# Optimization experiments

Measured on AMD Instinct MI355X. Metric: run time of the kernel, lower is better.

## Reference

```python
import jax, jax.numpy as jnp
import numpy as np
import math

H = 1024
E = 16
ENT_STRENGTH = 0.5
COHERENCE_TIME = 10.0
TIME_STEP = 0.0
K = 2
# static list of rotation pairs (i<j), applied sequentially as in the torch double loop
PAIRS = np.array([(i, j) for i in range(E) for j in range(i + 1, E)], dtype=np.int32)


def _mlp(x, w1, b1, w2, b2):
    h = jax.nn.gelu(x @ w1 + b1, approximate=False)  # torch default GELU = exact erf
    return h @ w2 + b2


def _apply_entanglement(amps, ent):
    # sequential Givens rotations over expert pairs; carry shape [B,S,E]
    pairs = jnp.asarray(PAIRS)

    def step(carry, pair):
        i, j = pair[0], pair[1]
        angle = ent[i, j] * ENT_STRENGTH
        c, s = jnp.cos(angle), jnp.sin(angle)
        ai = jnp.take(carry, i, axis=-1)  # [B,S]
        aj = jnp.take(carry, j, axis=-1)
        oh_i = jax.nn.one_hot(i, E, dtype=carry.dtype)
        oh_j = jax.nn.one_hot(j, E, dtype=carry.dtype)
        new = (carry * (1.0 - oh_i - oh_j)
               + (c * ai - s * aj)[..., None] * oh_i
               + (s * ai + c * aj)[..., None] * oh_j)
        return new, None

    out, _ = jax.lax.scan(step, amps, pairs)
    return out


def setup_inputs() -> dict:
    key = jax.random.key(0)
    ks = jax.random.split(key, 10)
    sc1 = 1.0 / math.sqrt(H)
    sc2 = 1.0 / math.sqrt(H // 2)
    return {
        "hidden_states": jax.random.normal(ks[0], (4, 4096, H), dtype=jnp.float32),
        "w1a": jax.random.uniform(ks[1], (H, H // 2), jnp.float32, -sc1, sc1),
        "b1a": jnp.zeros((H // 2,), jnp.float32),
        "w2a": jax.random.uniform(ks[2], (H // 2, E), jnp.float32, -sc2, sc2),
        "b2a": jnp.zeros((E,), jnp.float32),
        "w1p": jax.random.uniform(ks[3], (H, H // 2), jnp.float32, -sc1, sc1),
        "b1p": jnp.zeros((H // 2,), jnp.float32),
        "w2p": jax.random.uniform(ks[4], (H // 2, E), jnp.float32, -sc2, sc2),
        "b2p": jnp.zeros((E,), jnp.float32),
        "ent": jax.random.normal(ks[5], (E, E), dtype=jnp.float32) * 0.1,
    }


def reference(hidden_states, w1a, b1a, w2a, b2a, w1p, b1p, w2p, b2p, ent):
    raw_amps = _mlp(hidden_states, w1a, b1a, w2a, b2a)                 # [B,S,E]
    raw_phases = jnp.tanh(_mlp(hidden_states, w1p, b1p, w2p, b2p)) * jnp.float32(math.pi)
    amplitudes = jnp.sqrt(jax.nn.softmax(jnp.abs(raw_amps), axis=-1))
    entangled = _apply_entanglement(amplitudes, ent)
    coherence = jnp.exp(jnp.float32(-TIME_STEP / COHERENCE_TIME))      # time_step buffer = 0 -> 1.0
    decoherent = entangled * coherence
    probs = decoherent ** 2
    probs = probs / jnp.maximum(jnp.sum(jnp.abs(probs), axis=-1, keepdims=True), 1e-12)
    top_p, top_i = jax.lax.top_k(probs, K)
    top_p = top_p / jnp.maximum(jnp.sum(jnp.abs(top_p), axis=-1, keepdims=True), 1e-12)
    return top_p, top_i, decoherent, raw_phases, probs
```

## Files before the change

### kernel.cpp

```cpp
#include <hip/hip_runtime.h>
#include <math.h>

#define NTOK   16384
#define HDIM   1024
#define HHALF  512
#define NE     16

#define OFF_TP  0
#define OFF_TI  (NTOK * 2)
#define OFF_DEC (NTOK * 4)
#define OFF_PH  (OFF_DEC + NTOK * NE)
#define OFF_PR  (OFF_PH + NTOK * NE)

typedef _Float16 half8 __attribute__((ext_vector_type(8)));
typedef _Float16 half4 __attribute__((ext_vector_type(4)));
typedef float f32x16 __attribute__((ext_vector_type(16)));
typedef float f32x4 __attribute__((ext_vector_type(4)));

#define LO_SCALE     2048.0f
#define LO_SCALE_INV (1.0f / 2048.0f)
#define MFMA32(a,b,c) __builtin_amdgcn_mfma_f32_32x32x16_f16(a,b,c,0,0,0)
#define MFMA16(a,b,c) __builtin_amdgcn_mfma_f32_16x16x32_f16(a,b,c,0,0,0)

#define BAR() asm volatile("s_waitcnt lgkmcnt(0)\n\ts_barrier" ::: "memory")

__device__ __forceinline__ float gelu_exact(float x) {
    return 0.5f * x * (1.0f + erff(x * 0.70710678118654752440f));
}

__device__ __forceinline__ void cvt_split(float4 v, half4& hi, half4& lo) {
    _Float16 h0 = (_Float16)v.x, h1 = (_Float16)v.y,
             h2 = (_Float16)v.z, h3 = (_Float16)v.w;
    hi = (half4){h0, h1, h2, h3};
    lo = (half4){(_Float16)((v.x - (float)h0) * LO_SCALE),
                 (_Float16)((v.y - (float)h1) * LO_SCALE),
                 (_Float16)((v.z - (float)h2) * LO_SCALE),
                 (_Float16)((v.w - (float)h3) * LO_SCALE)};
}

__global__ void __launch_bounds__(256)
qir_wtrans(const float* __restrict__ w1a, const float* __restrict__ w1p,
           _Float16* __restrict__ wt, float* __restrict__ out)
{
    int u = blockIdx.x * 256 + threadIdx.x;
    out[OFF_PH + u] = 0.0f;
    out[OFF_PH + 262144 + u] = 0.0f;

    int l  = u & 63;
    int f  = (u >> 6) & 7;
    int sl = (u >> 9) & 7;
    int kc = (u >> 12) & 31;
    int ph = u >> 17;
    int nf = f >> 2, kh = (f >> 1) & 1, pl = f & 1;
    int col = sl * 64 + nf * 32 + (l & 31);
    int k0  = kc * 32 + kh * 16 + (l >> 5) * 8;
    const float* __restrict__ W = ph ? w1p : w1a;
    half8 v;
    #pragma unroll
    for (int j = 0; j < 8; ++j) {
        float x = W[(size_t)(k0 + j) * HHALF + col];
        _Float16 h = (_Float16)x;
        v[j] = pl ? (_Float16)((x - (float)h) * LO_SCALE) : h;
    }
    *(half8*)&wt[(size_t)u * 8] = v;
}

__device__ __forceinline__ void kstep(
    int kc, const float* __restrict__ aptr, const _Float16* __restrict__ bptr,
    char* Acur, char* Anxt, int a_rd, int a_off0, int a_off1,
    half8 (&Bc)[8], half8 (&Bn)[8],
    float4 (&xw)[2], float4 (&xl)[2],
    f32x16& a00, f32x16& a01, f32x16& a10, f32x16& a11,
    f32x16& c00, f32x16& c01, f32x16& c10, f32x16& c11)
{
    if (kc + 2 < 32) {
        xl[0] = *(const float4*)(aptr + (kc + 2) * 32);
        xl[1] = *(const float4*)(aptr + (kc + 2) * 32 + 16);
    }
    if (kc + 1 < 32) {
        #pragma unroll
        for (int f = 0; f < 8; ++f)
            Bn[f] = *(const half8*)(bptr + (size_t)(kc + 1) * 32768 + f * 512);
    }
    #pragma unroll
    for (int kh = 0; kh < 2; ++kh) {
        const char* Ah = Acur + kh * 2048 + a_rd;
        half8 ah0 = *(const half8*)(Ah);
        half8 ah1 = *(const half8*)(Ah + 512);
        half8 al0 = *(const half8*)(Ah + 4096);
        half8 al1 = *(const half8*)(Ah + 4096 + 512);
        half8 bh0 = Bc[kh * 2],     bl0 = Bc[kh * 2 + 1];
        half8 bh1 = Bc[4 + kh * 2], bl1 = Bc[4 + kh * 2 + 1];
        a00 = MFMA32(ah0, bh0, a00); c00 = MFMA32(al0, bh0, c00); c00 = MFMA32(ah0, bl0, c00);
        a01 = MFMA32(ah0, bh1, a01); c01 = MFMA32(al0, bh1, c01); c01 = MFMA32(ah0, bl1, c01);
        a10 = MFMA32(ah1, bh0, a10); c10 = MFMA32(al1, bh0, c10); c10 = MFMA32(ah1, bl0, c10);
        a11 = MFMA32(ah1, bh1, a11); c11 = MFMA32(al1, bh1, c11); c11 = MFMA32(ah1, bl1, c11);
    }
    if (kc + 1 < 32) {
        half4 hv, lv;
        cvt_split(xw[0], hv, lv);
        *(half4*)(Anxt + a_off0) = hv; *(half4*)(Anxt + a_off0 + 4096) = lv;
        cvt_split(xw[1], hv, lv);
        *(half4*)(Anxt + a_off1) = hv; *(half4*)(Anxt + a_off1 + 4096) = lv;
    }
    BAR();
}

__global__ void __launch_bounds__(256, 2)
qir_gemm(const float* __restrict__ xg, const _Float16* __restrict__ wt,
         const float* __restrict__ b1a, const float* __restrict__ w2a, const float* __restrict__ b2a,
         const float* __restrict__ b1p, const float* __restrict__ w2p, const float* __restrict__ b2p,
         float* __restrict__ out)
{
    extern __shared__ char smem[];
    const int tid = threadIdx.x;
    const int l  = tid & 63;
    const int w  = tid >> 6;
    const int bid  = blockIdx.x;
    const int mblk = bid & 255;
    const int v    = bid >> 8;
    const int ph   = v & 1;
    const int nh   = v >> 1;
    const int tok0 = mblk * 64;

    const float* __restrict__ b1 = ph ? b1p : b1a;
    const float* __restrict__ w2 = ph ? w2p : w2a;
    const float* __restrict__ b2 = ph ? b2p : b2a;
    const _Float16* __restrict__ wtp = wt + ((size_t)ph << 20);

    char* const Ab0 = smem;
    char* const Ab1 = smem + 8192;

    const int r  = tid >> 2;
    const int kq = tid & 3;
    const float* __restrict__ aptr = xg + (size_t)(tok0 + r) * HDIM + kq * 4;
    const int a_off0 = (kq >> 1) * 1024 + r * 16 + (kq & 1) * 8;
    const int a_off1 = a_off0 + 2048;
    const int a_rd = (l >> 5) * 1024 + (l & 31) * 16;

    const _Float16* __restrict__ bptr = wtp + (nh * 4 + w) * 4096 + (size_t)l * 8;

    f32x16 a00{}, a01{}, a10{}, a11{}, c00{}, c01{}, c10{}, c11{};
    #pragma unroll
    for (int rg = 0; rg < 16; ++rg) {
        a00[rg] = 0.f; a01[rg] = 0.f; a10[rg] = 0.f; a11[rg] = 0.f;
        c00[rg] = 0.f; c01[rg] = 0.f; c10[rg] = 0.f; c11[rg] = 0.f;
    }

    half8 Bc[8], Bn[8];
    float4 xw[2], xl[2];

    {
        float4 v0 = *(const float4*)(aptr);
        float4 v1 = *(const float4*)(aptr + 16);
        half4 hv, lv;
        cvt_split(v0, hv, lv);
        *(half4*)(Ab0 + a_off0) = hv; *(half4*)(Ab0 + a_off0 + 4096) = lv;
        cvt_split(v1, hv, lv);
        *(half4*)(Ab0 + a_off1) = hv; *(half4*)(Ab0 + a_off1 + 4096) = lv;
    }
    #pragma unroll
    for (int f = 0; f < 8; ++f) Bc[f] = *(const half8*)(bptr + f * 512);
    xw[0] = *(const float4*)(aptr + 32);
    xw[1] = *(const float4*)(aptr + 48);
    BAR();

    for (int kk = 0; kk < 16; ++kk) {
        kstep(2 * kk,     aptr, bptr, Ab0, Ab1, a_rd, a_off0, a_off1,
              Bc, Bn, xw, xl, a00, a01, a10, a11, c00, c01, c10, c11);
        kstep(2 * kk + 1, aptr, bptr, Ab1, Ab0, a_rd, a_off0, a_off1,
              Bn, Bc, xl, xw, a00, a01, a10, a11, c00, c01, c10, c11);
    }

    const int col0 = nh * 256 + w * 64 + (l & 31);
    const float bb0 = b1[col0], bb1 = b1[col0 + 32];
    #pragma unroll
    for (int rg = 0; rg < 16; ++rg) {
        a00[rg] = gelu_exact(a00[rg] + c00[rg] * LO_SCALE_INV + bb0);
        a01[rg] = gelu_exact(a01[rg] + c01[rg] * LO_SCALE_INV + bb1);
        a10[rg] = gelu_exact(a10[rg] + c10[rg] * LO_SCALE_INV + bb0);
        a11[rg] = gelu_exact(a11[rg] + c11[rg] * LO_SCALE_INV + bb1);
    }

    char* const Hw = smem + w * 4096;
    char* const hb = Hw + ((l >> 3) & 3) * 1024 + (l & 7) * 2;
    float* const P = (float*)(smem + 16384);

    half8 w2h[2], w2l[2];
    #pragma unroll
    for (int nf = 0; nf < 2; ++nf) {
        #pragma unroll
        for (int j = 0; j < 8; ++j) {
            int kg = nh * 256 + w * 64 + nf * 32 + (l >> 4) * 8 + j;
            float vv = w2[(size_t)kg * NE + (l & 15)];
            _Float16 hh = (_Float16)vv;
            w2h[nf][j] = hh;
            w2l[nf][j] = (_Float16)((vv - (float)hh) * LO_SCALE);
        }
    }

    f32x4 acc2[4], acc2s[4];
    #pragma unroll
    for (int m16 = 0; m16 < 4; ++m16)
        #pragma unroll
        for (int rg = 0; rg < 4; ++rg) { acc2[m16][rg] = 0.f; acc2s[m16][rg] = 0.f; }

#define H2PASS(ACC0, ACC1, NF, PL)                                             \
    {                                                                          \
        _Pragma("unroll")                                                      \
        for (int rg = 0; rg < 16; ++rg) {                                      \
            int row0 = (rg & 3) + 8 * (rg >> 2) + 4 * (l >> 5);                \
            { float vv = ACC0[rg]; _Float16 hh = (_Float16)vv;                 \
              *(_Float16*)(hb + row0 * 16) =                                   \
                  (PL) ? (_Float16)(vv - (float)hh) : hh; }                    \
            { float vv = ACC1[rg]; _Float16 hh = (_Float16)vv;                 \
              *(_Float16*)(hb + (32 + row0) * 16) =                            \
                  (PL) ? (_Float16)(vv - (float)hh) : hh; }                    \
        }                                                                      \
        _Pragma("unroll")                                                      \
        for (int m16 = 0; m16 < 4; ++m16) {                                    \
            half8 a2 = *(const half8*)(Hw + (l >> 4) * 1024 +                  \
                                       (m16 * 16 + (l & 15)) * 16);            \
            acc2[m16] = MFMA16(a2, w2h[NF], acc2[m16]);                        \
            if (!(PL)) acc2s[m16] = MFMA16(a2, w2l[NF], acc2s[m16]);           \
        }                                                                      \
    }

    H2PASS(a00, a10, 0, 0)
    H2PASS(a01, a11, 1, 0)
    H2PASS(a00, a10, 0, 1)
    H2PASS(a01, a11, 1, 1)
#undef H2PASS

    #pragma unroll
    for (int m16 = 0; m16 < 4; ++m16)
        #pragma unroll
        for (int rg = 0; rg < 4; ++rg) {
            int row = m16 * 16 + ((l >> 4) << 2) + rg;
            P[w * 1024 + row * 16 + (l & 15)] =
                acc2[m16][rg] + acc2s[m16][rg] * LO_SCALE_INV;
        }
    __syncthreads();

    #pragma unroll
    for (int rep = 0; rep < 4; ++rep) {
        int oi = tid + rep * 256;
        int t = oi >> 4, e = oi & 15;
        float sum = 0.5f * b2[e]
                  + P[0 * 1024 + t * 16 + e]
                  + P[1 * 1024 + t * 16 + e]
                  + P[2 * 1024 + t * 16 + e]
                  + P[3 * 1024 + t * 16 + e];
        atomicAdd(out + (ph ? OFF_PH : OFF_PR) + (size_t)(tok0 + t) * NE + e, sum);
    }
}

__global__ void __launch_bounds__(512)
qir_mlp(const float* __restrict__ xg,
        const float* __restrict__ w1a, const float* __restrict__ b1a,
        const float* __restrict__ w2a, const float* __restrict__ b2a,
        const float* __restrict__ w1p, const float* __restrict__ b1p,
        const float* __restrict__ w2p, const float* __restrict__ b2p,
        float* __restrict__ out)
{
    __shared__ float sh_w[16][HHALF];
    __shared__ float sh_x[16][68];

    const int tid  = threadIdx.x;
    const int cg   = tid & 63;
    const int tg   = tid >> 6;
    const int tok0 = blockIdx.x * 64;
    const int cA   = cg * 4;
    const int cB   = 256 + cg * 4;

    for (int phase = 0; phase < 2; ++phase) {
        const float* __restrict__ w1 = phase ? w1p : w1a;
        const float* __restrict__ b1 = phase ? b1p : b1a;
        const float* __restrict__ w2 = phase ? w2p : w2a;
        const float* __restrict__ b2 = phase ? b2p : b2a;

        float acc[8][8];
        #pragma unroll
        for (int t = 0; t < 8; ++t)
            #pragma unroll
            for (int c = 0; c < 8; ++c) acc[t][c] = 0.0f;

        float4 wreg[4];
        float4 xreg = make_float4(0.f, 0.f, 0.f, 0.f);

        auto load_chunk = [&](int kc) {
            #pragma unroll
            for (int p = 0; p < 4; ++p) {
                int f  = tid + p * 512;
                int k  = f >> 7;
                int c4 = (f & 127) << 2;
                wreg[p] = *(const float4*)&w1[(kc * 16 + k) * HHALF + c4];
            }
            if (tid < 256) {
                int t  = tid >> 2;
                int k4 = (tid & 3) << 2;
                xreg = *(const float4*)&xg[(size_t)(tok0 + t) * HDIM + kc * 16 + k4];
            }
        };

        load_chunk(0);
        for (int kc = 0; kc < HDIM / 16; ++kc) {
            __syncthreads();
            #pragma unroll
            for (int p = 0; p < 4; ++p) {
                int f  = tid + p * 512;
                int k  = f >> 7;
                int c4 = (f & 127) << 2;
                *(float4*)&sh_w[k][c4] = wreg[p];
            }
            if (tid < 256) {
                int t  = tid >> 2;
                int k4 = (tid & 3) << 2;
                sh_x[k4 + 0][t] = xreg.x;
                sh_x[k4 + 1][t] = xreg.y;
                sh_x[k4 + 2][t] = xreg.z;
                sh_x[k4 + 3][t] = xreg.w;
            }
            __syncthreads();
            if (kc + 1 < HDIM / 16) load_chunk(kc + 1);

            #pragma unroll 4
            for (int k = 0; k < 16; ++k) {
                float4 xa = *(const float4*)&sh_x[k][tg * 8];
                float4 xb = *(const float4*)&sh_x[k][tg * 8 + 4];
                float4 wa = *(const float4*)&sh_w[k][cA];
                float4 wb = *(const float4*)&sh_w[k][cB];
                float xs[8] = {xa.x, xa.y, xa.z, xa.w, xb.x, xb.y, xb.z, xb.w};
                float ws[8] = {wa.x, wa.y, wa.z, wa.w, wb.x, wb.y, wb.z, wb.w};
                #pragma unroll
                for (int t = 0; t < 8; ++t)
                    #pragma unroll
                    for (int c = 0; c < 8; ++c)
                        acc[t][c] = fmaf(xs[t], ws[c], acc[t][c]);
            }
        }

        {
            float4 bA4 = *(const float4*)&b1[cA];
            float4 bB4 = *(const float4*)&b1[cB];
            float bs[8] = {bA4.x, bA4.y, bA4.z, bA4.w, bB4.x, bB4.y, bB4.z, bB4.w};
            #pragma unroll
            for (int t = 0; t < 8; ++t)
                #pragma unroll
                for (int c = 0; c < 8; ++c)
                    acc[t][c] = gelu_exact(acc[t][c] + bs[c]);
        }

        for (int e = 0; e < NE; ++e) {
            float w2v[8];
            #pragma unroll
            for (int j = 0; j < 4; ++j) {
                w2v[j]     = w2[(cA + j) * NE + e];
                w2v[4 + j] = w2[(cB + j) * NE + e];
            }
            float bias2 = b2[e];
            #pragma unroll
            for (int t = 0; t < 8; ++t) {
                float s = 0.0f;
                #pragma unroll
                for (int j = 0; j < 8; ++j) s = fmaf(acc[t][j], w2v[j], s);
                #pragma unroll
                for (int off = 1; off < 64; off <<= 1)
                    s += __shfl_xor(s, off, 64);
                if (cg == 0) {
                    float raw   = s + bias2;
                    int   token = tok0 + tg * 8 + t;
                    out[(phase ? OFF_PH : OFF_PR) + (size_t)token * NE + e] = raw;
                }
            }
        }
    }
}

__global__ void __launch_bounds__(256)
qir_epilogue(const float* __restrict__ ent, float* __restrict__ out)
{
    __shared__ float sh_c[120], sh_s[120];
    const int tid = threadIdx.x;
    if (tid < 120) {
        int rem = tid, i = 0;
        while (rem >= 15 - i) { rem -= 15 - i; ++i; }
        int j = i + 1 + rem;
        float ang = ent[i * NE + j] * 0.5f;
        sh_c[tid] = cosf(ang);
        sh_s[tid] = sinf(ang);
    }
    __syncthreads();

    const int token = blockIdx.x * 256 + tid;

    #pragma unroll
    for (int q = 0; q < 4; ++q) {
        float4 v = *(const float4*)&out[OFF_PH + (size_t)token * NE + q * 4];
        v.x = tanhf(v.x) * 3.14159265358979323846f;
        v.y = tanhf(v.y) * 3.14159265358979323846f;
        v.z = tanhf(v.z) * 3.14159265358979323846f;
        v.w = tanhf(v.w) * 3.14159265358979323846f;
        *(float4*)&out[OFF_PH + (size_t)token * NE + q * 4] = v;
    }

    float a[16];
    #pragma unroll
    for (int q = 0; q < 4; ++q) {
        float4 v = *(const float4*)&out[OFF_PR + (size_t)token * NE + q * 4];
        a[q*4+0] = v.x; a[q*4+1] = v.y; a[q*4+2] = v.z; a[q*4+3] = v.w;
    }

    float m = fabsf(a[0]);
    #pragma unroll
    for (int e = 1; e < 16; ++e) m = fmaxf(m, fabsf(a[e]));
    float ssum = 0.0f;
    #pragma unroll
    for (int e = 0; e < 16; ++e) { a[e] = expf(fabsf(a[e]) - m); ssum += a[e]; }
    float inv = 1.0f / ssum;
    #pragma unroll
    for (int e = 0; e < 16; ++e) a[e] = sqrtf(a[e] * inv);

    {
        int p = 0;
        #pragma unroll
        for (int i = 0; i < 16; ++i) {
            #pragma unroll
            for (int j = i + 1; j < 16; ++j) {
                float c = sh_c[p], s = sh_s[p]; ++p;
                float ai = a[i], aj = a[j];
                a[i] = c * ai - s * aj;
                a[j] = s * ai + c * aj;
            }
        }
    }

    #pragma unroll
    for (int q = 0; q < 4; ++q)
        *(float4*)&out[OFF_DEC + (size_t)token * NE + q * 4] =
            make_float4(a[q*4], a[q*4+1], a[q*4+2], a[q*4+3]);

    float pr[16];
    float s2 = 0.0f;
    #pragma unroll
    for (int e = 0; e < 16; ++e) { pr[e] = a[e] * a[e]; s2 += pr[e]; }
    float inv2 = 1.0f / fmaxf(s2, 1e-12f);
    #pragma unroll
    for (int e = 0; e < 16; ++e) pr[e] *= inv2;
    #pragma unroll
    for (int q = 0; q < 4; ++q)
        *(float4*)&out[OFF_PR + (size_t)token * NE + q * 4] =
            make_float4(pr[q*4], pr[q*4+1], pr[q*4+2], pr[q*4+3]);

    float bv = pr[0]; int bi = 0;
    #pragma unroll
    for (int e = 1; e < 16; ++e) if (pr[e] > bv) { bv = pr[e]; bi = e; }
    float sv = -1.0f; int si = 0;
    #pragma unroll
    for (int e = 0; e < 16; ++e) if (e != bi && pr[e] > sv) { sv = pr[e]; si = e; }
    float ts = fmaxf(fabsf(bv) + fabsf(sv), 1e-12f);
    out[OFF_TP + (size_t)token * 2 + 0] = bv / ts;
    out[OFF_TP + (size_t)token * 2 + 1] = sv / ts;
    out[OFF_TI + (size_t)token * 2 + 0] = (float)bi;
    out[OFF_TI + (size_t)token * 2 + 1] = (float)si;
}

extern "C" void kernel_launch(void* const* d_in, const int* in_sizes, int n_in,
                              void* d_out, int out_size, void* d_ws, size_t ws_size,
                              hipStream_t stream) {
    const float* xg  = (const float*)d_in[0];
    const float* w1a = (const float*)d_in[1];
    const float* b1a = (const float*)d_in[2];
    const float* w2a = (const float*)d_in[3];
    const float* b2a = (const float*)d_in[4];
    const float* w1p = (const float*)d_in[5];
    const float* b1p = (const float*)d_in[6];
    const float* w2p = (const float*)d_in[7];
    const float* b2p = (const float*)d_in[8];
    const float* ent = (const float*)d_in[9];
    float* out = (float*)d_out;

    if (ws_size >= (size_t)4 * 1024 * 1024) {
        _Float16* wt = (_Float16*)d_ws;
        qir_wtrans<<<1024, 256, 0, stream>>>(w1a, w1p, wt, out);
        qir_gemm<<<1024, 256, 32768, stream>>>(xg, wt, b1a, w2a, b2a,
                                               b1p, w2p, b2p, out);
    } else {
        qir_mlp<<<NTOK / 64, 512, 0, stream>>>(xg, w1a, b1a, w2a, b2a,
                                               w1p, b1p, w2p, b2p, out);
    }
    qir_epilogue<<<NTOK / 256, 256, 0, stream>>>(ent, out);
}
```

Baseline: 125.9 us.

## Replace split-f16 GEMM scheme with f16/bf16 three-term product and narrower tiles

The first-layer GEMM changes its error-compensated split. Instead of hi/lo f16 terms on both operands with separate accumulators, it uses the x hi and scaled lo parts times the W f16 hi, plus a bf16 x-hi times a bf16 W residual. Everything accumulates into a single scaled accumulator pair per wave, and the lo-times-lo and separate correction accumulators are dropped. Each block now covers 32 columns per wave instead of 64, so the grid doubles to 2048 blocks, occupancy rises to 3 blocks per CU, and register pressure drops. The risks are reduced precision from the bf16 residual term and more total A-tile conversion and LDS traffic per output.

```diff
diff --git a/kernel.cpp b/kernel.cpp
--- a/kernel.cpp
+++ b/kernel.cpp
@@ -5,6 +5,7 @@
 #define HDIM   1024
 #define HHALF  512
 #define NE     16
+#define PI_F   3.14159265358979323846f
 
 #define OFF_TP  0
 #define OFF_TI  (NTOK * 2)
@@ -14,33 +15,31 @@
 
 typedef _Float16 half8 __attribute__((ext_vector_type(8)));
 typedef _Float16 half4 __attribute__((ext_vector_type(4)));
+typedef short    bf8   __attribute__((ext_vector_type(8)));
+typedef short    bf4   __attribute__((ext_vector_type(4)));
 typedef float f32x16 __attribute__((ext_vector_type(16)));
 typedef float f32x4 __attribute__((ext_vector_type(4)));
 
-#define LO_SCALE     2048.0f
-#define LO_SCALE_INV (1.0f / 2048.0f)
-#define MFMA32(a,b,c) __builtin_amdgcn_mfma_f32_32x32x16_f16(a,b,c,0,0,0)
-#define MFMA16(a,b,c) __builtin_amdgcn_mfma_f32_16x16x32_f16(a,b,c,0,0,0)
+#define SCALE      2048.0f
+#define SCALE_INV  (1.0f / 2048.0f)
+#define MFMA_F16(a,b,c)  __builtin_amdgcn_mfma_f32_32x32x16_f16(a,b,c,0,0,0)
+#define MFMA_BF16(a,b,c) __builtin_amdgcn_mfma_f32_32x32x16_bf16(a,b,c,0,0,0)
+#define MFMA16(a,b,c)    __builtin_amdgcn_mfma_f32_16x16x32_f16(a,b,c,0,0,0)
 
 #define BAR() asm volatile("s_waitcnt lgkmcnt(0)\n\ts_barrier" ::: "memory")
 
 __device__ __forceinline__ float gelu_exact(float x) {
     return 0.5f * x * (1.0f + erff(x * 0.70710678118654752440f));
 }
-
-__device__ __forceinline__ void cvt_split(float4 v, half4& hi, half4& lo) {
-    _Float16 h0 = (_Float16)v.x, h1 = (_Float16)v.y,
-             h2 = (_Float16)v.z, h3 = (_Float16)v.w;
-    hi = (half4){h0, h1, h2, h3};
-    lo = (half4){(_Float16)((v.x - (float)h0) * LO_SCALE),
-                 (_Float16)((v.y - (float)h1) * LO_SCALE),
-                 (_Float16)((v.z - (float)h2) * LO_SCALE),
-                 (_Float16)((v.w - (float)h3) * LO_SCALE)};
+__device__ __forceinline__ short f32_to_bf16_bits(float f) {
+    unsigned u = __builtin_bit_cast(unsigned, f);
+    u += 0x7FFFu + ((u >> 16) & 1u);
+    return (short)(u >> 16);
 }
 
 __global__ void __launch_bounds__(256)
 qir_wtrans(const float* __restrict__ w1a, const float* __restrict__ w1p,
-           _Float16* __restrict__ wt, float* __restrict__ out)
+           short* __restrict__ wt, float* __restrict__ out)
 {
     int u = blockIdx.x * 256 + threadIdx.x;
     out[OFF_PH + u] = 0.0f;
@@ -55,23 +54,23 @@
     int col = sl * 64 + nf * 32 + (l & 31);
     int k0  = kc * 32 + kh * 16 + (l >> 5) * 8;
     const float* __restrict__ W = ph ? w1p : w1a;
-    half8 v;
+    bf8 v;
     #pragma unroll
     for (int j = 0; j < 8; ++j) {
         float x = W[(size_t)(k0 + j) * HHALF + col];
         _Float16 h = (_Float16)x;
-        v[j] = pl ? (_Float16)((x - (float)h) * LO_SCALE) : h;
-    }
-    *(half8*)&wt[(size_t)u * 8] = v;
+        v[j] = pl ? f32_to_bf16_bits(x - (float)h)
+                  : __builtin_bit_cast(short, h);
+    }
+    *(bf8*)&wt[(size_t)u * 8] = v;
 }
 
 __device__ __forceinline__ void kstep(
-    int kc, const float* __restrict__ aptr, const _Float16* __restrict__ bptr,
-    char* Acur, char* Anxt, int a_rd, int a_off0, int a_off1,
-    half8 (&Bc)[8], half8 (&Bn)[8],
+    int kc, const float* __restrict__ aptr, const short* __restrict__ bptr,
+    char* Acur, char* Anxt, int a_rd, int a_w0,
+    bf8 (&Bc)[4], bf8 (&Bn)[4],
     float4 (&xw)[2], float4 (&xl)[2],
-    f32x16& a00, f32x16& a01, f32x16& a10, f32x16& a11,
-    f32x16& c00, f32x16& c01, f32x16& c10, f32x16& c11)
+    f32x16& acc0, f32x16& acc1)
 {
     if (kc + 2 < 32) {
         xl[0] = *(const float4*)(aptr + (kc + 2) * 32);
@@ -79,35 +78,55 @@
     }
     if (kc + 1 < 32) {
         #pragma unroll
-        for (int f = 0; f < 8; ++f)
-            Bn[f] = *(const half8*)(bptr + (size_t)(kc + 1) * 32768 + f * 512);
+        for (int j = 0; j < 4; ++j)
+            Bn[j] = *(const bf8*)(bptr + (size_t)(kc + 1) * 32768 + j * 512);
     }
     #pragma unroll
     for (int kh = 0; kh < 2; ++kh) {
-        const char* Ah = Acur + kh * 2048 + a_rd;
-        half8 ah0 = *(const half8*)(Ah);
-        half8 ah1 = *(const half8*)(Ah + 512);
-        half8 al0 = *(const half8*)(Ah + 4096);
-        half8 al1 = *(const half8*)(Ah + 4096 + 512);
-        half8 bh0 = Bc[kh * 2],     bl0 = Bc[kh * 2 + 1];
-        half8 bh1 = Bc[4 + kh * 2], bl1 = Bc[4 + kh * 2 + 1];
-        a00 = MFMA32(ah0, bh0, a00); c00 = MFMA32(al0, bh0, c00); c00 = MFMA32(ah0, bl0, c00);
-        a01 = MFMA32(ah0, bh1, a01); c01 = MFMA32(al0, bh1, c01); c01 = MFMA32(ah0, bl1, c01);
-        a10 = MFMA32(ah1, bh0, a10); c10 = MFMA32(al1, bh0, c10); c10 = MFMA32(ah1, bl0, c10);
-        a11 = MFMA32(ah1, bh1, a11); c11 = MFMA32(al1, bh1, c11); c11 = MFMA32(ah1, bl1, c11);
+        const char* Ah = Acur + kh * 6144 + a_rd;
+        half8 xh0 = *(const half8*)(Ah);
+        half8 xh1 = *(const half8*)(Ah + 512);
+        half8 xl0 = *(const half8*)(Ah + 1024);
+        half8 xl1 = *(const half8*)(Ah + 1536);
+        bf8   xb0 = *(const bf8*)  (Ah + 2048);
+        bf8   xb1 = *(const bf8*)  (Ah + 2560);
+        half8 wh  = __builtin_bit_cast(half8, Bc[kh * 2]);
+        bf8   wlo = Bc[kh * 2 + 1];
+        acc0 = MFMA_F16(xh0, wh, acc0);
+        acc1 = MFMA_F16(xh1, wh, acc1);
+        acc0 = MFMA_F16(xl0, wh, acc0);
+        acc1 = MFMA_F16(xl1, wh, acc1);
+        acc0 = MFMA_BF16(xb0, wlo, acc0);
+        acc1 = MFMA_BF16(xb1, wlo, acc1);
     }
     if (kc + 1 < 32) {
-        half4 hv, lv;
-        cvt_split(xw[0], hv, lv);
-        *(half4*)(Anxt + a_off0) = hv; *(half4*)(Anxt + a_off0 + 4096) = lv;
-        cvt_split(xw[1], hv, lv);
-        *(half4*)(Anxt + a_off1) = hv; *(half4*)(Anxt + a_off1 + 4096) = lv;
+        #pragma unroll
+        for (int kh = 0; kh < 2; ++kh) {
+            float4 v = kh ? xw[1] : xw[0];
+            _Float16 h0 = (_Float16)v.x, h1 = (_Float16)v.y,
+                     h2 = (_Float16)v.z, h3 = (_Float16)v.w;
+            const _Float16 S = (_Float16)SCALE;
+            half4 hi = {(_Float16)(h0 * S), (_Float16)(h1 * S),
+                        (_Float16)(h2 * S), (_Float16)(h3 * S)};
+            half4 lo = {(_Float16)((v.x - (float)h0) * SCALE),
+                        (_Float16)((v.y - (float)h1) * SCALE),
+                        (_Float16)((v.z - (float)h2) * SCALE),
+                        (_Float16)((v.w - (float)h3) * SCALE)};
+            bf4 hb = {f32_to_bf16_bits((float)h0 * SCALE),
+                      f32_to_bf16_bits((float)h1 * SCALE),
+                      f32_to_bf16_bits((float)h2 * SCALE),
+                      f32_to_bf16_bits((float)h3 * SCALE)};
+            char* base = Anxt + kh * 6144 + a_w0;
+            *(half4*)(base)        = hi;
+            *(half4*)(base + 1024) = lo;
+            *(bf4*)  (base + 2048) = hb;
+        }
     }
     BAR();
 }
 
-__global__ void __launch_bounds__(256, 2)
-qir_gemm(const float* __restrict__ xg, const _Float16* __restrict__ wt,
+__global__ void __launch_bounds__(256, 3)
+qir_gemm(const float* __restrict__ xg, const short* __restrict__ wt,
          const float* __restrict__ b1a, const float* __restrict__ w2a, const float* __restrict__ b2a,
          const float* __restrict__ b1p, const float* __restrict__ w2p, const float* __restrict__ b2p,
          float* __restrict__ out)
@@ -126,77 +145,83 @@
     const float* __restrict__ b1 = ph ? b1p : b1a;
     const float* __restrict__ w2 = ph ? w2p : w2a;
     const float* __restrict__ b2 = ph ? b2p : b2a;
-    const _Float16* __restrict__ wtp = wt + ((size_t)ph << 20);
+    const short* __restrict__ wtp = wt + ((size_t)ph << 20);
 
     char* const Ab0 = smem;
-    char* const Ab1 = smem + 8192;
+    char* const Ab1 = smem + 12288;
 
     const int r  = tid >> 2;
     const int kq = tid & 3;
     const float* __restrict__ aptr = xg + (size_t)(tok0 + r) * HDIM + kq * 4;
-    const int a_off0 = (kq >> 1) * 1024 + r * 16 + (kq & 1) * 8;
-    const int a_off1 = a_off0 + 2048;
-    const int a_rd = (l >> 5) * 1024 + (l & 31) * 16;
-
-    const _Float16* __restrict__ bptr = wtp + (nh * 4 + w) * 4096 + (size_t)l * 8;
-
-    f32x16 a00{}, a01{}, a10{}, a11{}, c00{}, c01{}, c10{}, c11{};
-    #pragma unroll
-    for (int rg = 0; rg < 16; ++rg) {
-        a00[rg] = 0.f; a01[rg] = 0.f; a10[rg] = 0.f; a11[rg] = 0.f;
-        c00[rg] = 0.f; c01[rg] = 0.f; c10[rg] = 0.f; c11[rg] = 0.f;
-    }
-
-    half8 Bc[8], Bn[8];
-    float4 xw[2], xl[2];
+    const int a_w0 = (kq >> 1) * 3072 + r * 16 + (kq & 1) * 8;
+    const int a_rd = (l >> 5) * 3072 + (l & 31) * 16;
+
+    const int c32 = nh * 4 + w;
+    const short* __restrict__ bptr =
+        wtp + ((size_t)(c32 >> 1) * 8 + (size_t)(c32 & 1) * 4) * 512 + (size_t)l * 8;
+
+    f32x16 acc0{}, acc1{};
+    #pragma unroll
+    for (int rg = 0; rg < 16; ++rg) { acc0[rg] = 0.f; acc1[rg] = 0.f; }
+
+    bf8 Bc[4], Bn[4];
+    float4 xw[2], xl4[2];
 
     {
-        float4 v0 = *(const float4*)(aptr);
-        float4 v1 = *(const float4*)(aptr + 16);
-        half4 hv, lv;
-        cvt_split(v0, hv, lv);
-        *(half4*)(Ab0 + a_off0) = hv; *(half4*)(Ab0 + a_off0 + 4096) = lv;
-        cvt_split(v1, hv, lv);
-        *(half4*)(Ab0 + a_off1) = hv; *(half4*)(Ab0 + a_off1 + 4096) = lv;
-    }
-    #pragma unroll
-    for (int f = 0; f < 8; ++f) Bc[f] = *(const half8*)(bptr + f * 512);
+        #pragma unroll
+        for (int kh = 0; kh < 2; ++kh) {
+            float4 vv = *(const float4*)(aptr + kh * 16);
+            _Float16 h0 = (_Float16)vv.x, h1 = (_Float16)vv.y,
+                     h2 = (_Float16)vv.z, h3 = (_Float16)vv.w;
+            const _Float16 S = (_Float16)SCALE;
+            half4 hi = {(_Float16)(h0 * S), (_Float16)(h1 * S),
+                        (_Float16)(h2 * S), (_Float16)(h3 * S)};
+            half4 lo = {(_Float16)((vv.x - (float)h0) * SCALE),
+                        (_Float16)((vv.y - (float)h1) * SCALE),
+                        (_Float16)((vv.z - (float)h2) * SCALE),
+                        (_Float16)((vv.w - (float)h3) * SCALE)};
+            bf4 hb = {f32_to_bf16_bits((float)h0 * SCALE),
+                      f32_to_bf16_bits((float)h1 * SCALE),
+                      f32_to_bf16_bits((float)h2 * SCALE),
+                      f32_to_bf16_bits((float)h3 * SCALE)};
+            char* base = Ab0 + kh * 6144 + a_w0;
+            *(half4*)(base)        = hi;
+            *(half4*)(base + 1024) = lo;
+            *(bf4*)  (base + 2048) = hb;
+        }
+    }
+    #pragma unroll
+    for (int j = 0; j < 4; ++j) Bc[j] = *(const bf8*)(bptr + j * 512);
     xw[0] = *(const float4*)(aptr + 32);
     xw[1] = *(const float4*)(aptr + 48);
     BAR();
 
     for (int kk = 0; kk < 16; ++kk) {
-        kstep(2 * kk,     aptr, bptr, Ab0, Ab1, a_rd, a_off0, a_off1,
-              Bc, Bn, xw, xl, a00, a01, a10, a11, c00, c01, c10, c11);
-        kstep(2 * kk + 1, aptr, bptr, Ab1, Ab0, a_rd, a_off0, a_off1,
-              Bn, Bc, xl, xw, a00, a01, a10, a11, c00, c01, c10, c11);
-    }
-
-    const int col0 = nh * 256 + w * 64 + (l & 31);
-    const float bb0 = b1[col0], bb1 = b1[col0 + 32];
+        kstep(2 * kk,     aptr, bptr, Ab0, Ab1, a_rd, a_w0,
+              Bc, Bn, xw, xl4, acc0, acc1);
+        kstep(2 * kk + 1, aptr, bptr, Ab1, Ab0, a_rd, a_w0,
+              Bn, Bc, xl4, xw, acc0, acc1);
+    }
+
+    const float bb = b1[nh * 128 + w * 32 + (l & 31)];
     #pragma unroll
     for (int rg = 0; rg < 16; ++rg) {
-        a00[rg] = gelu_exact(a00[rg] + c00[rg] * LO_SCALE_INV + bb0);
-        a01[rg] = gelu_exact(a01[rg] + c01[rg] * LO_SCALE_INV + bb1);
-        a10[rg] = gelu_exact(a10[rg] + c10[rg] * LO_SCALE_INV + bb0);
-        a11[rg] = gelu_exact(a11[rg] + c11[rg] * LO_SCALE_INV + bb1);
+        acc0[rg] = gelu_exact(acc0[rg] * SCALE_INV + bb);
+        acc1[rg] = gelu_exact(acc1[rg] * SCALE_INV + bb);
     }
 
     char* const Hw = smem + w * 4096;
     char* const hb = Hw + ((l >> 3) & 3) * 1024 + (l & 7) * 2;
     float* const P = (float*)(smem + 16384);
 
-    half8 w2h[2], w2l[2];
-    #pragma unroll
-    for (int nf = 0; nf < 2; ++nf) {
-        #pragma unroll
-        for (int j = 0; j < 8; ++j) {
-            int kg = nh * 256 + w * 64 + nf * 32 + (l >> 4) * 8 + j;
-            float vv = w2[(size_t)kg * NE + (l & 15)];
-            _Float16 hh = (_Float16)vv;
-            w2h[nf][j] = hh;
-            w2l[nf][j] = (_Float16)((vv - (float)hh) * LO_SCALE);
-        }
+    half8 w2h, w2l;
+    #pragma unroll
+    for (int j = 0; j < 8; ++j) {
+        int kg = nh * 128 + w * 32 + (l >> 4) * 8 + j;
+        float vv = w2[(size_t)kg * NE + (l & 15)];
+        _Float16 hh = (_Float16)vv;
+        w2h[j] = hh;
+        w2l[j] = (_Float16)((vv - (float)hh) * SCALE);
     }
 
     f32x4 acc2[4], acc2s[4];
@@ -205,32 +230,33 @@
         #pragma unroll
         for (int rg = 0; rg < 4; ++rg) { acc2[m16][rg] = 0.f; acc2s[m16][rg] = 0.f; }
 
-#define H2PASS(ACC0, ACC1, NF, PL)                                             \
-    {                                                                          \
-        _Pragma("unroll")                                                      \
-        for (int rg = 0; rg < 16; ++rg) {                                      \
-            int row0 = (rg & 3) + 8 * (rg >> 2) + 4 * (l >> 5);                \
-            { float vv = ACC0[rg]; _Float16 hh = (_Float16)vv;                 \
-              *(_Float16*)(hb + row0 * 16) =                                   \
-                  (PL) ? (_Float16)(vv - (float)hh) : hh; }                    \
-            { float vv = ACC1[rg]; _Float16 hh = (_Float16)vv;                 \
-              *(_Float16*)(hb + (32 + row0) * 16) =                            \
-                  (PL) ? (_Float16)(vv - (float)hh) : hh; }                    \
-        }                                                                      \
-        _Pragma("unroll")                                                      \
-        for (int m16 = 0; m16 < 4; ++m16) {                                    \
-            half8 a2 = *(const half8*)(Hw + (l >> 4) * 1024 +                  \
-                                       (m16 * 16 + (l & 15)) * 16);            \
-            acc2[m16] = MFMA16(a2, w2h[NF], acc2[m16]);                        \
-            if (!(PL)) acc2s[m16] = MFMA16(a2, w2l[NF], acc2s[m16]);           \
-        }                                                                      \
-    }
-
-    H2PASS(a00, a10, 0, 0)
-    H2PASS(a01, a11, 1, 0)
-    H2PASS(a00, a10, 0, 1)
-    H2PASS(a01, a11, 1, 1)
-#undef H2PASS
+    #pragma unroll
+    for (int rg = 0; rg < 16; ++rg) {
+        int row0 = (rg & 3) + 8 * (rg >> 2) + 4 * (l >> 5);
+        *(_Float16*)(hb + row0 * 16)        = (_Float16)acc0[rg];
+        *(_Float16*)(hb + (32 + row0) * 16) = (_Float16)acc1[rg];
+    }
+    #pragma unroll
+    for (int m16 = 0; m16 < 4; ++m16) {
+        half8 a2 = *(const half8*)(Hw + (l >> 4) * 1024 +
+                                   (m16 * 16 + (l & 15)) * 16);
+        acc2[m16]  = MFMA16(a2, w2h, acc2[m16]);
+        acc2s[m16] = MFMA16(a2, w2l, acc2s[m16]);
+    }
+    #pragma unroll
+    for (int rg = 0; rg < 16; ++rg) {
+        int row0 = (rg & 3) + 8 * (rg >> 2) + 4 * (l >> 5);
+        { float vv = acc0[rg]; _Float16 hh = (_Float16)vv;
+          *(_Float16*)(hb + row0 * 16) = (_Float16)(vv - (float)hh); }
+        { float vv = acc1[rg]; _Float16 hh = (_Float16)vv;
+          *(_Float16*)(hb + (32 + row0) * 16) = (_Float16)(vv - (float)hh); }
+    }
+    #pragma unroll
+    for (int m16 = 0; m16 < 4; ++m16) {
+        half8 a2 = *(const half8*)(Hw + (l >> 4) * 1024 +
+                                   (m16 * 16 + (l & 15)) * 16);
+        acc2[m16] = MFMA16(a2, w2h, acc2[m16]);
+    }
 
     #pragma unroll
     for (int m16 = 0; m16 < 4; ++m16)
@@ -238,7 +264,7 @@
         for (int rg = 0; rg < 4; ++rg) {
             int row = m16 * 16 + ((l >> 4) << 2) + rg;
             P[w * 1024 + row * 16 + (l & 15)] =
-                acc2[m16][rg] + acc2s[m16][rg] * LO_SCALE_INV;
+                acc2[m16][rg] + acc2s[m16][rg] * SCALE_INV;
         }
     __syncthreads();
 
@@ -246,7 +272,7 @@
     for (int rep = 0; rep < 4; ++rep) {
         int oi = tid + rep * 256;
         int t = oi >> 4, e = oi & 15;
-        float sum = 0.5f * b2[e]
+        float sum = 0.25f * b2[e]
                   + P[0 * 1024 + t * 16 + e]
                   + P[1 * 1024 + t * 16 + e]
                   + P[2 * 1024 + t * 16 + e]
@@ -397,10 +423,10 @@
     #pragma unroll
     for (int q = 0; q < 4; ++q) {
         float4 v = *(const float4*)&out[OFF_PH + (size_t)token * NE + q * 4];
-        v.x = tanhf(v.x) * 3.14159265358979323846f;
-        v.y = tanhf(v.y) * 3.14159265358979323846f;
-        v.z = tanhf(v.z) * 3.14159265358979323846f;
-        v.w = tanhf(v.w) * 3.14159265358979323846f;
+        v.x = tanhf(v.x) * PI_F;
+        v.y = tanhf(v.y) * PI_F;
+        v.z = tanhf(v.z) * PI_F;
+        v.w = tanhf(v.w) * PI_F;
         *(float4*)&out[OFF_PH + (size_t)token * NE + q * 4] = v;
     }
 
@@ -481,9 +507,9 @@
     float* out = (float*)d_out;
 
     if (ws_size >= (size_t)4 * 1024 * 1024) {
-        _Float16* wt = (_Float16*)d_ws;
+        short* wt = (short*)d_ws;
         qir_wtrans<<<1024, 256, 0, stream>>>(w1a, w1p, wt, out);
-        qir_gemm<<<1024, 256, 32768, stream>>>(xg, wt, b1a, w2a, b2a,
+        qir_gemm<<<2048, 256, 32768, stream>>>(xg, wt, b1a, w2a, b2a,
                                                b1p, w2p, b2p, out);
     } else {
         qir_mlp<<<NTOK / 64, 512, 0, stream>>>(xg, w1a, b1a, w2a, b2a,
```

Result: slower. 144.5 us (+14.8%).
